# Kernel optimization log

Measured on AMD Instinct MI355X. Metric: run time of the kernel, lower is better.

The kernel has to match this reference:

```python
import jax, jax.numpy as jnp
import numpy as np

# Fixed LeNet C3 connection table: input channel i feeds these 10 output channels.
CONN = [[0, 4, 5, 6, 9, 10, 11, 12, 14, 15],
        [0, 1, 5, 6, 7, 10, 11, 12, 13, 15],
        [0, 1, 2, 6, 7, 8, 11, 13, 14, 15],
        [1, 2, 3, 6, 7, 8, 9, 12, 14, 15],
        [2, 3, 4, 7, 8, 9, 10, 12, 13, 15],
        [3, 4, 5, 8, 9, 10, 11, 13, 14, 15]]
# Static scatter indices: (out_channel, in_channel) pairs, 60 total.
_ROWS = np.concatenate([np.asarray(l, np.int32) for l in CONN])  # out-channel ids
_COLS = np.repeat(np.arange(6, dtype=np.int32), 10)              # in-channel ids


def setup_inputs() -> dict:
    key = jax.random.key(0)
    k1, k2 = jax.random.split(key)
    x = jax.random.normal(k1, (64, 6, 256, 256), jnp.float32)
    # kaiming-uniform-ish scale for 6*5*5 fan-in
    weight = jax.random.normal(k2, (10, 6, 5, 5), jnp.float32) * 0.1
    bias = jnp.full((1, 16, 1, 1), 0.01, jnp.float32)
    return {"x": x, "weight": weight, "bias": bias}


def reference(x, weight, bias):
    # Fold the per-input-channel loop + scatter-add into one dense [16,6,5,5]
    # kernel with zeros where the connection table is absent. Each iteration i
    # of the original adds conv(x[:,i], weight[j,i]) to out channel CONN[i][j].
    w_flat = weight.transpose(1, 0, 2, 3).reshape(60, 5, 5)  # ordered (i, j)
    w_full = jnp.zeros((16, 6, 5, 5), weight.dtype).at[_ROWS, _COLS].set(w_flat)
    # Bias for channel c is added once per list containing c -> multiply by count.
    counts = jnp.zeros((16,), weight.dtype).at[_ROWS].add(1.0)
    out = jax.lax.conv_general_dilated(
        x, w_full, window_strides=(1, 1), padding='VALID',
        dimension_numbers=('NCHW', 'OIHW', 'NCHW'))
    return out + bias * counts.reshape(1, 16, 1, 1)
```

## Files before the change

kernel.cpp:

```cpp
#include <hip/hip_runtime.h>
#include <hip/hip_fp16.h>

typedef _Float16 f16x8 __attribute__((ext_vector_type(8)));
typedef float f32x16 __attribute__((ext_vector_type(16)));

__device__ constexpr int CONN[6][10] = {
    {0, 4, 5, 6, 9, 10, 11, 12, 14, 15},
    {0, 1, 5, 6, 7, 10, 11, 12, 13, 15},
    {0, 1, 2, 6, 7, 8, 11, 13, 14, 15},
    {1, 2, 3, 6, 7, 8, 9, 12, 14, 15},
    {2, 3, 4, 7, 8, 9, 10, 12, 13, 15},
    {3, 4, 5, 8, 9, 10, 11, 13, 14, 15}};

__device__ constexpr int CNT[16] = {3,3,3,3,3,3,4,4,4,4,4,4,4,4,4,6};

__device__ __forceinline__ f16x8 u4_to_h8(uint4 u) { f16x8 r; __builtin_memcpy(&r, &u, 16); return r; }

#define PITCH_DW 132
#define PLANE_DW 2128
#define LDS_DW   (6 * 2128 + 140)

__global__ void prep_A(const float* __restrict__ w, unsigned short* __restrict__ Wp) {
    int t = blockIdx.x * 256 + threadIdx.x;
    if (t >= 7680) return;
    int j = t & 7, lane = (t >> 3) & 63, ms = t >> 9;
    int ch = lane & 31, kb = lane >> 5;
    int slice = ms + 15 * kb;
    int ii = slice / 5, r = slice % 5;
    float val = 0.f;
    if (ch < 16 && j < 5)
        for (int jj = 0; jj < 10; ++jj)
            if (CONN[ii][jj] == ch) val = w[jj * 150 + ii * 25 + r * 5 + j];
    __half h = __float2half(val);
    unsigned short u; __builtin_memcpy(&u, &h, 2);
    Wp[t] = u;
}

__global__ __launch_bounds__(256, 3) void c3_mfma(
    const float* __restrict__ x, const unsigned short* __restrict__ Wp,
    const float* __restrict__ bias, float* __restrict__ out)
{
    __shared__ unsigned s_lds[LDS_DW];

    const int tid = threadIdx.x;
    const int id = (blockIdx.x & 7) * 168 + (blockIdx.x >> 3);
    const int by = id % 21;
    const int n  = id / 21;
    const int Y0 = by * 12;
    const float* xin = x + (size_t)n * 6 * 65536;

    #pragma unroll 4
    for (int it = 0; it < 24; ++it) {
        int i   = tid + it * 256;
        int c4  = i & 63;
        int row = (i >> 6) & 15;
        int ch  = i >> 10;
        float4 v = *reinterpret_cast<const float4*>(
            xin + (size_t)ch * 65536 + (size_t)(Y0 + row) * 256 + c4 * 4);
        __half2 lo = __floats2half2_rn(v.x, v.y);
        __half2 hi = __floats2half2_rn(v.z, v.w);
        uint2 u; __builtin_memcpy(&u.x, &lo, 4); __builtin_memcpy(&u.y, &hi, 4);
        *reinterpret_cast<uint2*>(&s_lds[ch * PLANE_DW + row * PITCH_DW + c4 * 2]) = u;
    }
    if (tid < 96) {
        int ch = tid >> 4, row = tid & 15;
        *reinterpret_cast<uint4*>(&s_lds[ch * PLANE_DW + row * PITCH_DW + 128]) =
            make_uint4(0u, 0u, 0u, 0u);
    }
    __syncthreads();

    const int lane = tid & 63;
    const int wv   = tid >> 6;
    const int nn   = lane & 31;
    const int kb   = lane >> 5;

    f16x8 W[15];
    const uint4* wp4 = reinterpret_cast<const uint4*>(Wp);
    #pragma unroll
    for (int ms = 0; ms < 15; ++ms) W[ms] = u4_to_h8(wp4[ms * 64 + lane]);

    f32x16 cinit;
    #pragma unroll
    for (int reg = 0; reg < 8; ++reg) {
        int ch = (reg & 3) + 8 * (reg >> 2) + 4 * kb;
        cinit[reg] = bias[ch] * (float)CNT[ch];
    }
    #pragma unroll
    for (int reg = 8; reg < 16; ++reg) cinit[reg] = 0.f;

    const unsigned shb = (unsigned)((nn & 1) * 16);

#define MFMA32(a, b, c) __builtin_amdgcn_mfma_f32_32x32x16_f16(a, b, c, 0, 0, 0)

    #pragma unroll 1
    for (int st = 0; st < 2; ++st) {
        const int gx  = (st * 4 + wv) * 32 + nn;
        const bool xok = gx < 252;
        const int pb  = 3 * kb * PLANE_DW + (gx >> 1);

        auto loadf = [&](int dw) -> f16x8 {
            int d0 = dw & ~1;
            uint2 r0 = *reinterpret_cast<const uint2*>(&s_lds[d0]);
            uint2 r1 = *reinterpret_cast<const uint2*>(&s_lds[d0 + 2]);
            uint2 r2 = *reinterpret_cast<const uint2*>(&s_lds[d0 + 4]);
            const bool odd = dw & 1;
            unsigned e0 = odd ? r0.y : r0.x;
            unsigned e1 = odd ? r1.x : r0.y;
            unsigned e2 = odd ? r1.y : r1.x;
            unsigned e3 = odd ? r2.x : r1.y;
            unsigned e4 = odd ? r2.y : r2.x;
            unsigned o0 = (unsigned)((((unsigned long long)e1 << 32) | e0) >> shb);
            unsigned o1 = (unsigned)((((unsigned long long)e2 << 32) | e1) >> shb);
            unsigned o2 = (unsigned)((((unsigned long long)e3 << 32) | e2) >> shb);
            unsigned o3 = (unsigned)((((unsigned long long)e4 << 32) | e3) >> shb);
            return u4_to_h8(make_uint4(o0, o1, o2, o3));
        };

        f16x8 F00 = loadf(pb + 0 * PITCH_DW), F01 = loadf(pb + 1 * PITCH_DW),
              F02 = loadf(pb + 2 * PITCH_DW), F03 = loadf(pb + 3 * PITCH_DW),
              F04 = loadf(pb + 4 * PITCH_DW);
        f16x8 F10 = loadf(pb + PLANE_DW + 0 * PITCH_DW), F11 = loadf(pb + PLANE_DW + 1 * PITCH_DW),
              F12 = loadf(pb + PLANE_DW + 2 * PITCH_DW), F13 = loadf(pb + PLANE_DW + 3 * PITCH_DW),
              F14 = loadf(pb + PLANE_DW + 4 * PITCH_DW);
        f16x8 F20 = loadf(pb + 2 * PLANE_DW + 0 * PITCH_DW), F21 = loadf(pb + 2 * PLANE_DW + 1 * PITCH_DW),
              F22 = loadf(pb + 2 * PLANE_DW + 2 * PITCH_DW), F23 = loadf(pb + 2 * PLANE_DW + 3 * PITCH_DW),
              F24 = loadf(pb + 2 * PLANE_DW + 4 * PITCH_DW);
        int rowN = 5 * PITCH_DW;

        float* const opg = out + (size_t)n * 16 * 63504 + (size_t)(4 * kb) * 63504 + gx;
        int yoff = Y0 * 252;

#define PHASE(f00,f01,f02,f03,f04, f10,f11,f12,f13,f14, f20,f21,f22,f23,f24)   \
    {                                                                          \
        f32x16 acc = cinit;                                                    \
        acc = MFMA32(W[0],  f00, acc);  acc = MFMA32(W[1],  f01, acc);         \
        acc = MFMA32(W[2],  f02, acc);  acc = MFMA32(W[3],  f03, acc);         \
        acc = MFMA32(W[4],  f04, acc);                                         \
        acc = MFMA32(W[5],  f10, acc);  acc = MFMA32(W[6],  f11, acc);         \
        acc = MFMA32(W[7],  f12, acc);  acc = MFMA32(W[8],  f13, acc);         \
        acc = MFMA32(W[9],  f14, acc);                                         \
        acc = MFMA32(W[10], f20, acc);  acc = MFMA32(W[11], f21, acc);         \
        acc = MFMA32(W[12], f22, acc);  acc = MFMA32(W[13], f23, acc);         \
        acc = MFMA32(W[14], f24, acc);                                         \
        if (xok) {                                                             \
            opg[yoff +  0 * 63504] = acc[0];                                   \
            opg[yoff +  1 * 63504] = acc[1];                                   \
            opg[yoff +  2 * 63504] = acc[2];                                   \
            opg[yoff +  3 * 63504] = acc[3];                                   \
            opg[yoff +  8 * 63504] = acc[4];                                   \
            opg[yoff +  9 * 63504] = acc[5];                                   \
            opg[yoff + 10 * 63504] = acc[6];                                   \
            opg[yoff + 11 * 63504] = acc[7];                                   \
        }                                                                      \
        yoff += 252;                                                           \
        f00 = loadf(pb + rowN);                                                \
        f10 = loadf(pb + PLANE_DW + rowN);                                     \
        f20 = loadf(pb + 2 * PLANE_DW + rowN);                                 \
        rowN += PITCH_DW;                                                      \
    }

        PHASE(F00,F01,F02,F03,F04, F10,F11,F12,F13,F14, F20,F21,F22,F23,F24)
        PHASE(F01,F02,F03,F04,F00, F11,F12,F13,F14,F10, F21,F22,F23,F24,F20)
        PHASE(F02,F03,F04,F00,F01, F12,F13,F14,F10,F11, F22,F23,F24,F20,F21)
        PHASE(F03,F04,F00,F01,F02, F13,F14,F10,F11,F12, F23,F24,F20,F21,F22)
        PHASE(F04,F00,F01,F02,F03, F14,F10,F11,F12,F13, F24,F20,F21,F22,F23)
        PHASE(F00,F01,F02,F03,F04, F10,F11,F12,F13,F14, F20,F21,F22,F23,F24)
        PHASE(F01,F02,F03,F04,F00, F11,F12,F13,F14,F10, F21,F22,F23,F24,F20)
        PHASE(F02,F03,F04,F00,F01, F12,F13,F14,F10,F11, F22,F23,F24,F20,F21)
        PHASE(F03,F04,F00,F01,F02, F13,F14,F10,F11,F12, F23,F24,F20,F21,F22)
        PHASE(F04,F00,F01,F02,F03, F14,F10,F11,F12,F13, F24,F20,F21,F22,F23)
        PHASE(F00,F01,F02,F03,F04, F10,F11,F12,F13,F14, F20,F21,F22,F23,F24)
        PHASE(F01,F02,F03,F04,F00, F11,F12,F13,F14,F10, F21,F22,F23,F24,F20)
#undef PHASE
    }
#undef MFMA32
}

extern "C" void kernel_launch(void* const* d_in, const int* in_sizes, int n_in,
                              void* d_out, int out_size, void* d_ws, size_t ws_size,
                              hipStream_t stream) {
    const float* x    = (const float*)d_in[0];
    const float* w    = (const float*)d_in[1];
    const float* bias = (const float*)d_in[2];
    float* out = (float*)d_out;
    unsigned short* Wp = (unsigned short*)d_ws;

    hipLaunchKernelGGL(prep_A, dim3(30), dim3(256), 0, stream, w, Wp);
    hipLaunchKernelGGL(c3_mfma, dim3(1344), dim3(256), 0, stream, x, Wp, bias, out);
}
```

Before: 116.5 us.

## Fuse weight-panel prep into conv kernel and retile to 21-row strips

Drops the separate prep_A launch: each block now builds the fp16 weight panel in shared memory and loads its MFMA A-operands from there. Retiles so each 512-thread block covers a 21-output-row by full-width strip, with 8 waves each owning 32 columns. This removes the two-pass column loop and cuts the redundant halo-row input reads from 16/12 to 25/21 per output row. The costs are redundant per-block weight-panel construction and a 92 KB dynamic LDS footprint that limits residency to two blocks per CU. Right-edge row reads now spill into the next row instead of a zeroed pad, which is safe only because those lanes' outputs are masked or multiplied by zero weights.

```diff
diff --git a/kernel.cpp b/kernel.cpp
--- a/kernel.cpp
+++ b/kernel.cpp
@@ -16,56 +16,50 @@
 
 __device__ __forceinline__ f16x8 u4_to_h8(uint4 u) { f16x8 r; __builtin_memcpy(&r, &u, 16); return r; }
 
-#define PITCH_DW 132
-#define PLANE_DW 2128
-#define LDS_DW   (6 * 2128 + 140)
+#define PITCH_DW 128
+#define PLANE_DW 3200
+#define SIN_DW   19200
+#define LDS_DW   (19200 + 3840)
 
-__global__ void prep_A(const float* __restrict__ w, unsigned short* __restrict__ Wp) {
-    int t = blockIdx.x * 256 + threadIdx.x;
-    if (t >= 7680) return;
-    int j = t & 7, lane = (t >> 3) & 63, ms = t >> 9;
-    int ch = lane & 31, kb = lane >> 5;
-    int slice = ms + 15 * kb;
-    int ii = slice / 5, r = slice % 5;
-    float val = 0.f;
-    if (ch < 16 && j < 5)
-        for (int jj = 0; jj < 10; ++jj)
-            if (CONN[ii][jj] == ch) val = w[jj * 150 + ii * 25 + r * 5 + j];
-    __half h = __float2half(val);
-    unsigned short u; __builtin_memcpy(&u, &h, 2);
-    Wp[t] = u;
-}
-
-__global__ __launch_bounds__(256, 3) void c3_mfma(
-    const float* __restrict__ x, const unsigned short* __restrict__ Wp,
+__global__ __launch_bounds__(512, 2) void c3_mfma(
+    const float* __restrict__ x, const float* __restrict__ w,
     const float* __restrict__ bias, float* __restrict__ out)
 {
-    __shared__ unsigned s_lds[LDS_DW];
+    extern __shared__ unsigned s_lds[];
+    unsigned short* s_panel = reinterpret_cast<unsigned short*>(s_lds + SIN_DW);
 
     const int tid = threadIdx.x;
-    const int id = (blockIdx.x & 7) * 168 + (blockIdx.x >> 3);
-    const int by = id % 21;
-    const int n  = id / 21;
-    const int Y0 = by * 12;
+    const int id = (blockIdx.x & 7) * 96 + (blockIdx.x >> 3);
+    const int by = id % 12;
+    const int n  = id / 12;
+    const int Y0 = by * 21;
     const float* xin = x + (size_t)n * 6 * 65536;
 
-    #pragma unroll 4
-    for (int it = 0; it < 24; ++it) {
-        int i   = tid + it * 256;
+    for (int t = tid; t < 7680; t += 512) {
+        int j = t & 7, lane = (t >> 3) & 63, ms = t >> 9;
+        int ch = lane & 31, kb = lane >> 5;
+        int slice = ms + 15 * kb;
+        int ii = slice / 5, r = slice % 5;
+        float val = 0.f;
+        if (ch < 16 && j < 5)
+            for (int jj = 0; jj < 10; ++jj)
+                if (CONN[ii][jj] == ch) val = w[jj * 150 + ii * 25 + r * 5 + j];
+        __half h = __float2half(val);
+        unsigned short u; __builtin_memcpy(&u, &h, 2);
+        s_panel[t] = u;
+    }
+
+    for (int i = tid; i < 9600; i += 512) {
         int c4  = i & 63;
-        int row = (i >> 6) & 15;
-        int ch  = i >> 10;
+        int t   = i >> 6;
+        int ch  = t / 25;
+        int row = t - ch * 25;
         float4 v = *reinterpret_cast<const float4*>(
             xin + (size_t)ch * 65536 + (size_t)(Y0 + row) * 256 + c4 * 4);
         __half2 lo = __floats2half2_rn(v.x, v.y);
         __half2 hi = __floats2half2_rn(v.z, v.w);
         uint2 u; __builtin_memcpy(&u.x, &lo, 4); __builtin_memcpy(&u.y, &hi, 4);
         *reinterpret_cast<uint2*>(&s_lds[ch * PLANE_DW + row * PITCH_DW + c4 * 2]) = u;
-    }
-    if (tid < 96) {
-        int ch = tid >> 4, row = tid & 15;
-        *reinterpret_cast<uint4*>(&s_lds[ch * PLANE_DW + row * PITCH_DW + 128]) =
-            make_uint4(0u, 0u, 0u, 0u);
     }
     __syncthreads();
 
@@ -75,9 +69,11 @@
     const int kb   = lane >> 5;
 
     f16x8 W[15];
-    const uint4* wp4 = reinterpret_cast<const uint4*>(Wp);
-    #pragma unroll
-    for (int ms = 0; ms < 15; ++ms) W[ms] = u4_to_h8(wp4[ms * 64 + lane]);
+    {
+        const uint4* p4 = reinterpret_cast<const uint4*>(s_panel);
+        #pragma unroll
+        for (int ms = 0; ms < 15; ++ms) W[ms] = u4_to_h8(p4[ms * 64 + lane]);
+    }
 
     f32x16 cinit;
     #pragma unroll
@@ -88,47 +84,44 @@
     #pragma unroll
     for (int reg = 8; reg < 16; ++reg) cinit[reg] = 0.f;
 
+    const int gx  = 32 * wv + nn;
+    const bool ok = gx < 252;
+    const int pb  = 3 * kb * PLANE_DW + (gx >> 1);
+    const bool odd = (gx >> 1) & 1;
     const unsigned shb = (unsigned)((nn & 1) * 16);
 
+    auto loadf = [&](int dw) -> f16x8 {
+        int d0 = dw & ~1;
+        uint2 r0 = *reinterpret_cast<const uint2*>(&s_lds[d0]);
+        uint2 r1 = *reinterpret_cast<const uint2*>(&s_lds[d0 + 2]);
+        uint2 r2 = *reinterpret_cast<const uint2*>(&s_lds[d0 + 4]);
+        unsigned e0 = odd ? r0.y : r0.x;
+        unsigned e1 = odd ? r1.x : r0.y;
+        unsigned e2 = odd ? r1.y : r1.x;
+        unsigned e3 = odd ? r2.x : r1.y;
+        unsigned e4 = odd ? r2.y : r2.x;
+        unsigned o0 = (unsigned)((((unsigned long long)e1 << 32) | e0) >> shb);
+        unsigned o1 = (unsigned)((((unsigned long long)e2 << 32) | e1) >> shb);
+        unsigned o2 = (unsigned)((((unsigned long long)e3 << 32) | e2) >> shb);
+        unsigned o3 = (unsigned)((((unsigned long long)e4 << 32) | e3) >> shb);
+        return u4_to_h8(make_uint4(o0, o1, o2, o3));
+    };
+
+    f16x8 F00 = loadf(pb + 0*PITCH_DW), F01 = loadf(pb + 1*PITCH_DW),
+          F02 = loadf(pb + 2*PITCH_DW), F03 = loadf(pb + 3*PITCH_DW),
+          F04 = loadf(pb + 4*PITCH_DW);
+    f16x8 F10 = loadf(pb + PLANE_DW + 0*PITCH_DW), F11 = loadf(pb + PLANE_DW + 1*PITCH_DW),
+          F12 = loadf(pb + PLANE_DW + 2*PITCH_DW), F13 = loadf(pb + PLANE_DW + 3*PITCH_DW),
+          F14 = loadf(pb + PLANE_DW + 4*PITCH_DW);
+    f16x8 F20 = loadf(pb + 2*PLANE_DW + 0*PITCH_DW), F21 = loadf(pb + 2*PLANE_DW + 1*PITCH_DW),
+          F22 = loadf(pb + 2*PLANE_DW + 2*PITCH_DW), F23 = loadf(pb + 2*PLANE_DW + 3*PITCH_DW),
+          F24 = loadf(pb + 2*PLANE_DW + 4*PITCH_DW);
+    int rowOff = 5 * PITCH_DW;
+
+    float* const opg = out + (size_t)n * 16 * 63504 + (size_t)(4 * kb) * 63504 + gx;
+    int yoff = Y0 * 252;
+
 #define MFMA32(a, b, c) __builtin_amdgcn_mfma_f32_32x32x16_f16(a, b, c, 0, 0, 0)
-
-    #pragma unroll 1
-    for (int st = 0; st < 2; ++st) {
-        const int gx  = (st * 4 + wv) * 32 + nn;
-        const bool xok = gx < 252;
-        const int pb  = 3 * kb * PLANE_DW + (gx >> 1);
-
-        auto loadf = [&](int dw) -> f16x8 {
-            int d0 = dw & ~1;
-            uint2 r0 = *reinterpret_cast<const uint2*>(&s_lds[d0]);
-            uint2 r1 = *reinterpret_cast<const uint2*>(&s_lds[d0 + 2]);
-            uint2 r2 = *reinterpret_cast<const uint2*>(&s_lds[d0 + 4]);
-            const bool odd = dw & 1;
-            unsigned e0 = odd ? r0.y : r0.x;
-            unsigned e1 = odd ? r1.x : r0.y;
-            unsigned e2 = odd ? r1.y : r1.x;
-            unsigned e3 = odd ? r2.x : r1.y;
-            unsigned e4 = odd ? r2.y : r2.x;
-            unsigned o0 = (unsigned)((((unsigned long long)e1 << 32) | e0) >> shb);
-            unsigned o1 = (unsigned)((((unsigned long long)e2 << 32) | e1) >> shb);
-            unsigned o2 = (unsigned)((((unsigned long long)e3 << 32) | e2) >> shb);
-            unsigned o3 = (unsigned)((((unsigned long long)e4 << 32) | e3) >> shb);
-            return u4_to_h8(make_uint4(o0, o1, o2, o3));
-        };
-
-        f16x8 F00 = loadf(pb + 0 * PITCH_DW), F01 = loadf(pb + 1 * PITCH_DW),
-              F02 = loadf(pb + 2 * PITCH_DW), F03 = loadf(pb + 3 * PITCH_DW),
-              F04 = loadf(pb + 4 * PITCH_DW);
-        f16x8 F10 = loadf(pb + PLANE_DW + 0 * PITCH_DW), F11 = loadf(pb + PLANE_DW + 1 * PITCH_DW),
-              F12 = loadf(pb + PLANE_DW + 2 * PITCH_DW), F13 = loadf(pb + PLANE_DW + 3 * PITCH_DW),
-              F14 = loadf(pb + PLANE_DW + 4 * PITCH_DW);
-        f16x8 F20 = loadf(pb + 2 * PLANE_DW + 0 * PITCH_DW), F21 = loadf(pb + 2 * PLANE_DW + 1 * PITCH_DW),
-              F22 = loadf(pb + 2 * PLANE_DW + 2 * PITCH_DW), F23 = loadf(pb + 2 * PLANE_DW + 3 * PITCH_DW),
-              F24 = loadf(pb + 2 * PLANE_DW + 4 * PITCH_DW);
-        int rowN = 5 * PITCH_DW;
-
-        float* const opg = out + (size_t)n * 16 * 63504 + (size_t)(4 * kb) * 63504 + gx;
-        int yoff = Y0 * 252;
 
 #define PHASE(f00,f01,f02,f03,f04, f10,f11,f12,f13,f14, f20,f21,f22,f23,f24)   \
     {                                                                          \
@@ -142,7 +135,7 @@
         acc = MFMA32(W[10], f20, acc);  acc = MFMA32(W[11], f21, acc);         \
         acc = MFMA32(W[12], f22, acc);  acc = MFMA32(W[13], f23, acc);         \
         acc = MFMA32(W[14], f24, acc);                                         \
-        if (xok) {                                                             \
+        if (ok) {                                                              \
             opg[yoff +  0 * 63504] = acc[0];                                   \
             opg[yoff +  1 * 63504] = acc[1];                                   \
             opg[yoff +  2 * 63504] = acc[2];                                   \
@@ -152,27 +145,29 @@
             opg[yoff + 10 * 63504] = acc[6];                                   \
             opg[yoff + 11 * 63504] = acc[7];                                   \
         }                                                                      \
-        yoff += 252;                                                           \
-        f00 = loadf(pb + rowN);                                                \
-        f10 = loadf(pb + PLANE_DW + rowN);                                     \
-        f20 = loadf(pb + 2 * PLANE_DW + rowN);                                 \
-        rowN += PITCH_DW;                                                      \
+        f00 = loadf(pb + rowOff);                                              \
+        f10 = loadf(pb + PLANE_DW + rowOff);                                   \
+        f20 = loadf(pb + 2 * PLANE_DW + rowOff);                               \
+        rowOff += PITCH_DW; yoff += 252;                                       \
     }
 
-        PHASE(F00,F01,F02,F03,F04, F10,F11,F12,F13,F14, F20,F21,F22,F23,F24)
-        PHASE(F01,F02,F03,F04,F00, F11,F12,F13,F14,F10, F21,F22,F23,F24,F20)
-        PHASE(F02,F03,F04,F00,F01, F12,F13,F14,F10,F11, F22,F23,F24,F20,F21)
-        PHASE(F03,F04,F00,F01,F02, F13,F14,F10,F11,F12, F23,F24,F20,F21,F22)
-        PHASE(F04,F00,F01,F02,F03, F14,F10,F11,F12,F13, F24,F20,F21,F22,F23)
-        PHASE(F00,F01,F02,F03,F04, F10,F11,F12,F13,F14, F20,F21,F22,F23,F24)
-        PHASE(F01,F02,F03,F04,F00, F11,F12,F13,F14,F10, F21,F22,F23,F24,F20)
-        PHASE(F02,F03,F04,F00,F01, F12,F13,F14,F10,F11, F22,F23,F24,F20,F21)
-        PHASE(F03,F04,F00,F01,F02, F13,F14,F10,F11,F12, F23,F24,F20,F21,F22)
-        PHASE(F04,F00,F01,F02,F03, F14,F10,F11,F12,F13, F24,F20,F21,F22,F23)
-        PHASE(F00,F01,F02,F03,F04, F10,F11,F12,F13,F14, F20,F21,F22,F23,F24)
-        PHASE(F01,F02,F03,F04,F00, F11,F12,F13,F14,F10, F21,F22,F23,F24,F20)
+#define P0 PHASE(F00,F01,F02,F03,F04, F10,F11,F12,F13,F14, F20,F21,F22,F23,F24)
+#define P1 PHASE(F01,F02,F03,F04,F00, F11,F12,F13,F14,F10, F21,F22,F23,F24,F20)
+#define P2 PHASE(F02,F03,F04,F00,F01, F12,F13,F14,F10,F11, F22,F23,F24,F20,F21)
+#define P3 PHASE(F03,F04,F00,F01,F02, F13,F14,F10,F11,F12, F23,F24,F20,F21,F22)
+#define P4 PHASE(F04,F00,F01,F02,F03, F14,F10,F11,F12,F13, F24,F20,F21,F22,F23)
+
+    P0 P1 P2 P3 P4
+    P0 P1 P2 P3 P4
+    P0 P1 P2 P3 P4
+    P0 P1 P2 P3 P4
+    P0
+#undef P0
+#undef P1
+#undef P2
+#undef P3
+#undef P4
 #undef PHASE
-    }
 #undef MFMA32
 }
 
@@ -183,8 +178,10 @@
     const float* w    = (const float*)d_in[1];
     const float* bias = (const float*)d_in[2];
     float* out = (float*)d_out;
-    unsigned short* Wp = (unsigned short*)d_ws;
 
-    hipLaunchKernelGGL(prep_A, dim3(30), dim3(256), 0, stream, w, Wp);
-    hipLaunchKernelGGL(c3_mfma, dim3(1344), dim3(256), 0, stream, x, Wp, bias, out);
+    static_assert(LDS_DW * 4 == 92160, "LDS size");
+    hipFuncSetAttribute(reinterpret_cast<const void*>(c3_mfma),
+                        hipFuncAttributeMaxDynamicSharedMemorySize, LDS_DW * 4);
+    hipLaunchKernelGGL(c3_mfma, dim3(768), dim3(512), LDS_DW * 4, stream,
+                       x, w, bias, out);
 }
```

After: 175.7 us. 1.51x slower.
